# Performance work log

Measured on AMD Instinct MI355X. Metric: run time of the kernel, lower is better.

## Reference

```python
import math
import jax, jax.numpy as jnp
import numpy as np

SR = 48000
FRAME = 240
TWO_PI = 2.0 * math.pi


def _forward(B_inh, f0_offset, A0, tau1, tau2, a1, beat_hz, beat_depth, noise,
             f0, width_factor, duration_s):
    n_samples = int(duration_s * SR)
    T = int(math.ceil(n_samples / FRAME)) * FRAME
    Bb, K = A0.shape

    # --- inharmonic partial frequencies ---
    f0_adj = f0 * 2.0 ** (f0_offset / 1200.0)                      # (B,)
    k = jnp.arange(1, K + 1, dtype=f0.dtype)                       # (K,)
    f_k = f0_adj[:, None] * k[None, :] * jnp.sqrt(1.0 + B_inh[:, None] * k[None, :] ** 2)
    f_kb = f_k + beat_hz                                           # (B,K)

    t = jnp.arange(T, dtype=f0.dtype) / SR                         # (T,)

    # --- two-stage exponential amplitude envelope, (B,K,T) ---
    env = A0[:, :, None] * (a1[:, :, None] * jnp.exp(-t / tau1[:, :, None])
                            + (1.0 - a1[:, :, None]) * jnp.exp(-t / tau2[:, :, None]))

    # fixed random phases (original uses a seeded generator)
    pk = jax.random.split(jax.random.key(42), 3)
    phi_m = jax.random.uniform(pk[0], (Bb, K)) * TWO_PI
    phi_b = jax.random.uniform(pk[1], (Bb, K)) * TWO_PI

    osc = (jnp.cos(TWO_PI * f_k[:, :, None] * t + phi_m[:, :, None])
           + beat_depth[:, :, None] * jnp.cos(TWO_PI * f_kb[:, :, None] * t + phi_b[:, :, None]))

    harmonic = jnp.sum(env * osc, axis=1)                          # (B,T)
    peak = jnp.clip(jnp.max(jnp.abs(harmonic), axis=1, keepdims=True), 1e-6, None)
    harmonic = harmonic / peak * 0.9

    # --- coloured noise: one-pole IIR via parallel associative scan ---
    attack_tau = noise[:, 0:1]                                     # (B,1)
    floor_rms = noise[:, 1:2]                                      # (B,1)
    centroid = noise[:, 2]                                         # (B,)
    nyq = SR / 2.0
    f_lo = 27.5
    log_range = math.log2(nyq / f_lo)
    cutoff = jnp.clip(f_lo * 2.0 ** (centroid * log_range) / nyq, 0.01, 0.99)
    pole = jnp.exp(-TWO_PI * cutoff)                               # (B,)
    alpha = 1.0 - pole

    white = jax.random.normal(pk[2], (Bb, T), dtype=f0.dtype)
    # x_i = pole * x_{i-1} + alpha * w_i  -> affine composition scan over time
    a = jnp.broadcast_to(pole[None, :], (T, Bb))                   # (T,B)
    b = alpha[None, :] * white.T                                   # (T,B)

    def comb(x, y):
        return (x[0] * y[0], x[1] * y[0] + y[1])

    _, filt = jax.lax.associative_scan(comb, (a, b), axis=0)
    noise_env = jnp.exp(-t[None, :] / jnp.clip(attack_tau, 0.002, None)) * floor_rms
    noise_sig = filt.T * noise_env                                 # (B,T)

    mono = (harmonic + noise_sig)[:, :n_samples]
    w = jnp.clip(width_factor, 0.0, 2.0)[:, None]
    side = mono * w * 0.3
    left = jnp.clip(mono + side, -1.0, 1.0)
    right = jnp.clip(mono - side, -1.0, 1.0)
    return jnp.stack([left, right], axis=1)                        # (B,2,n_samples)


def setup_inputs() -> dict:
    key = jax.random.key(0)
    B, K = 4, 64
    ks = jax.random.split(key, 12)
    f0 = jax.random.uniform(ks[0], (B,), minval=65.0, maxval=880.0)
    B_inh = jax.random.uniform(ks[1], (B,)) * 1e-4          # piano inharmonicity
    f0_offset = jax.random.normal(ks[2], (B,)) * 5.0        # cents
    A0 = jax.random.uniform(ks[3], (B, K))
    tau1 = jax.random.uniform(ks[4], (B, K)) * 0.4 + 0.05   # fast decay (s)
    tau2 = jax.random.uniform(ks[5], (B, K)) * 2.0 + 0.5    # slow decay (s)
    a1 = jax.random.uniform(ks[6], (B, K))
    beat_hz = jax.random.uniform(ks[7], (B, K)) * 2.0
    beat_depth = jax.random.uniform(ks[8], (B, K)) * 0.3
    noise = jnp.stack([
        jax.random.uniform(ks[9], (B,)) * 0.1 + 0.01,   # attack_tau
        jax.random.uniform(ks[10], (B,)) * 0.01,        # floor_rms
        jax.random.uniform(ks[11], (B,)),               # centroid_norm
        jnp.zeros((B,)),                                # slope_db_oct (unused)
    ], axis=1)
    width_factor = jnp.ones((B,))
    return dict(B_inh=B_inh, f0_offset=f0_offset, A0=A0, tau1=tau1, tau2=tau2,
                a1=a1, beat_hz=beat_hz, beat_depth=beat_depth, noise=noise,
                f0=f0, width_factor=width_factor, duration_s=3)


def reference(B_inh, f0_offset, A0, tau1, tau2, a1, beat_hz, beat_depth, noise,
              f0, width_factor, duration_s):
    return _forward(B_inh, f0_offset, A0, tau1, tau2, a1, beat_hz, beat_depth,
                    noise, f0, width_factor, duration_s)
```

## Files before the change

### kernel.cpp

```cpp
#include <hip/hip_runtime.h>
#include <stdint.h>
#include <math.h>

#pragma clang fp contract(off)

#define B_BATCH 4
#define K_HARM  64
#define T_TOT   144000
#define N_SAMP  144000
#define WF      128

#define OFF_PK    0
#define PK_STRIDE 16
#define OFF_POLE  4096
#define OFF_ALPHA 4100
#define OFF_AT    4104
#define OFF_FR    4108
#define OFF_WC    4112
#define OFF_PEAK  4116
#define OFF_HARM  4128

static constexpr float  TWO_PI_F = 6.28318530717958647692f;
static constexpr double INV2PI_D = 0.15915494309189535;
static constexpr float  C_HI = (float)INV2PI_D;
static constexpr float  C_LO = (float)(INV2PI_D - (double)((float)INV2PI_D));
static constexpr float  LOG2E_F = 1.44269504088896340736f;
static constexpr float  LN2_F   = 0.69314718055994530942f;

__device__ __forceinline__ uint32_t rotl32(uint32_t x, uint32_t n) {
    return (x << n) | (x >> (32u - n));
}

__device__ __forceinline__ void tf2x32(uint32_t k0, uint32_t k1, uint32_t x0, uint32_t x1,
                                       uint32_t& o0, uint32_t& o1) {
    const uint32_t ks2 = k0 ^ k1 ^ 0x1BD11BDAu;
    x0 += k0; x1 += k1;
#define TF_RND(r) { x0 += x1; x1 = rotl32(x1, (r)); x1 ^= x0; }
    TF_RND(13) TF_RND(15) TF_RND(26) TF_RND(6)
    x0 += k1;  x1 += ks2 + 1u;
    TF_RND(17) TF_RND(29) TF_RND(16) TF_RND(24)
    x0 += ks2; x1 += k0 + 2u;
    TF_RND(13) TF_RND(15) TF_RND(26) TF_RND(6)
    x0 += k0;  x1 += k1 + 3u;
    TF_RND(17) TF_RND(29) TF_RND(16) TF_RND(24)
    x0 += k1;  x1 += ks2 + 4u;
    TF_RND(13) TF_RND(15) TF_RND(26) TF_RND(6)
    x0 += ks2; x1 += k0 + 5u;
#undef TF_RND
    o0 = x0; o1 = x1;
}

__device__ __forceinline__ void get_keys(uint32_t pk[3][2]) {
    tf2x32(0u, 42u, 0u, 0u, pk[0][0], pk[0][1]);
    tf2x32(0u, 42u, 0u, 1u, pk[1][0], pk[1][1]);
    tf2x32(0u, 42u, 0u, 2u, pk[2][0], pk[2][1]);
}

__device__ __forceinline__ uint32_t bits_for(const uint32_t key[2], uint32_t idx) {
    uint32_t o0, o1;
    tf2x32(key[0], key[1], 0u, idx, o0, o1);
    return o0 ^ o1;
}

__device__ __forceinline__ float u01_from_bits(uint32_t bits) {
    return __fsub_rn(__uint_as_float((bits >> 9) | 0x3f800000u), 1.0f);
}

__device__ __forceinline__ float erfinv_fast(float x) {
    float v = fmaf(-x, x, 1.0f);
    float w = __fmul_rn(-LN2_F, __builtin_amdgcn_logf(v));
    float p;
    if (w < 5.0f) {
        w = __fsub_rn(w, 2.5f);
        p = 2.81022636e-08f;
        p = fmaf(p, w, 3.43273939e-07f);
        p = fmaf(p, w, -3.5233877e-06f);
        p = fmaf(p, w, -4.39150654e-06f);
        p = fmaf(p, w, 0.00021858087f);
        p = fmaf(p, w, -0.00125372503f);
        p = fmaf(p, w, -0.00417768164f);
        p = fmaf(p, w, 0.246640727f);
        p = fmaf(p, w, 1.50140941f);
    } else {
        w = __fsub_rn(sqrtf(w), 3.0f);
        p = -0.000200214257f;
        p = fmaf(p, w, 0.000100950558f);
        p = fmaf(p, w, 0.00134934322f);
        p = fmaf(p, w, -0.00367342844f);
        p = fmaf(p, w, 0.00573950773f);
        p = fmaf(p, w, -0.0076224613f);
        p = fmaf(p, w, 0.00943887047f);
        p = fmaf(p, w, 1.00167406f);
        p = fmaf(p, w, 2.83297682f);
    }
    return __fmul_rn(p, x);
}

__device__ __forceinline__ float normal_from_bits(uint32_t bits) {
    const float LO = __uint_as_float(0xBF7FFFFFu);
    float f = u01_from_bits(bits);
    float u = __fadd_rn(__fmul_rn(f, 2.0f), LO);
    u = fmaxf(u, LO);
    const float SQRT2_F = 1.41421356237309504880f;
    return __fmul_rn(SQRT2_F, erfinv_fast(u));
}

__device__ __forceinline__ float reduce_rev(float arg) {
    float p = __fmul_rn(arg, C_HI);
    float e = fmaf(arg, C_HI, -p);
    float n = rintf(p);
    float r = __fadd_rn(__fsub_rn(p, n), e);
    return fmaf(arg, C_LO, r);
}

__global__ void kprep(const float* __restrict__ B_inh, const float* __restrict__ f0_off,
                      const float* __restrict__ beat_hz, const float* __restrict__ noise,
                      const float* __restrict__ f0, const float* __restrict__ wfac,
                      const float* __restrict__ A0, const float* __restrict__ tau1,
                      const float* __restrict__ tau2, const float* __restrict__ a1,
                      const float* __restrict__ bd,
                      float* __restrict__ ws) {
    int j = threadIdx.x;
    uint32_t pk[3][2];
    get_keys(pk);

    float phim = __fmul_rn(u01_from_bits(bits_for(pk[0], (uint32_t)j)), TWO_PI_F);
    float phib = __fmul_rn(u01_from_bits(bits_for(pk[1], (uint32_t)j)), TWO_PI_F);

    int b = j >> 6;
    int k = (j & 63) + 1;
    float x   = __fdiv_rn(f0_off[b], 1200.0f);
    float s   = (float)exp2((double)x);
    float f0a = __fmul_rn(f0[b], s);
    float sq  = sqrtf(__fadd_rn(1.0f, __fmul_rn(B_inh[b], (float)(k * k))));
    float fk  = __fmul_rn(__fmul_rn(f0a, (float)k), sq);
    float fkb = __fadd_rn(fk, beat_hz[j]);

    float w_  = __fmul_rn(TWO_PI_F, fk);
    float wb_ = __fmul_rn(TWO_PI_F, fkb);
    float c1  = __fdiv_rn(-LOG2E_F, __fmul_rn(48000.0f, tau1[j]));
    float c2  = __fdiv_rn(-LOG2E_F, __fmul_rn(48000.0f, tau2[j]));

    float* P = ws + OFF_PK + j * PK_STRIDE;
    P[0] = w_;
    P[1] = wb_;
    P[2] = phim;
    P[3] = phib;
    P[4] = c1;
    P[5] = c2;
    float a1v = a1[j];
    P[6] = __fmul_rn(A0[j], a1v);
    P[7] = __fmul_rn(A0[j], __fsub_rn(1.0f, a1v));
    P[8] = bd[j];
    float revm = __fdiv_rn(fk,  48000.0f); revm = __fsub_rn(revm, floorf(revm));
    float revb = __fdiv_rn(fkb, 48000.0f); revb = __fsub_rn(revb, floorf(revb));
    P[9]  = __builtin_amdgcn_cosf(revm);
    P[10] = __builtin_amdgcn_sinf(revm);
    P[11] = __builtin_amdgcn_cosf(revb);
    P[12] = __builtin_amdgcn_sinf(revb);
    P[13] = __builtin_amdgcn_exp2f(c1);
    P[14] = __builtin_amdgcn_exp2f(c2);

    if (j < B_BATCH) {
        float at  = fmaxf(noise[j * 4 + 0], 0.002f);
        float fr  = noise[j * 4 + 1];
        float cen = noise[j * 4 + 2];
        float lr  = (float)log2(24000.0 / 27.5);
        float y   = __fmul_rn(cen, lr);
        float e   = (float)exp2((double)y);
        float v   = __fdiv_rn(__fmul_rn(27.5f, e), 24000.0f);
        float cut = fminf(fmaxf(v, 0.01f), 0.99f);
        float pole = expf(__fmul_rn(-TWO_PI_F, cut));
        ws[OFF_POLE + j]  = pole;
        ws[OFF_ALPHA + j] = __fsub_rn(1.0f, pole);
        ws[OFF_AT + j] = at;
        ws[OFF_FR + j] = fr;
        ws[OFF_WC + j] = fminf(fmaxf(wfac[j], 0.0f), 2.0f);
        ((unsigned int*)ws)[OFF_PEAK + j] = 0u;
    }
}

#define SPT_H 16
#define TBLK  1024
#define KQ_N  8
#define RROW  1056

__global__ void kharm(const float* __restrict__ prm,
                      float* __restrict__ harm,
                      unsigned int* __restrict__ peak) {
    __shared__ float red[KQ_N][RROW];
    __shared__ float mxs[KQ_N];
    const int tid  = threadIdx.x;
    const int lane = tid & 63;
    const int kq   = __builtin_amdgcn_readfirstlane(tid >> 6);
    const int b    = blockIdx.y;
    const int t0b  = blockIdx.x * TBLK;
    const int t0   = t0b + lane * SPT_H;

    const float fn0 = (float)t0;
    const float tt0 = __fdiv_rn(fn0, 48000.0f);

    float acc[SPT_H];
#pragma unroll
    for (int j = 0; j < SPT_H; ++j) acc[j] = 0.0f;

    const float* Pb = prm + OFF_PK + (((b << 6) + (kq << 3)) * PK_STRIDE);

#pragma unroll 2
    for (int kk = 0; kk < K_HARM / KQ_N; ++kk) {
        const float* P = Pb + kk * PK_STRIDE;
        float w  = P[0], wb2 = P[1], pm = P[2], pb = P[3];
        float c1 = P[4], c2 = P[5], A1 = P[6], A2 = P[7], bdk = P[8];
        float cdm = P[9], sdm = P[10], cdb = P[11], sdb = P[12];
        float d1 = P[13], d2 = P[14];

        float am = __fadd_rn(__fmul_rn(w,   tt0), pm);
        float ab = __fadd_rn(__fmul_rn(wb2, tt0), pb);
        float rm = reduce_rev(am);
        float rb = reduce_rev(ab);
        float cm = __builtin_amdgcn_cosf(rm), sm = __builtin_amdgcn_sinf(rm);
        float cb = __builtin_amdgcn_cosf(rb), sb = __builtin_amdgcn_sinf(rb);

        float xm  = cm;
        float xpm = fmaf(sm, sdm, __fmul_rn(cm, cdm));
        float xb  = __fmul_rn(bdk, cb);
        float xpb = __fmul_rn(bdk, fmaf(sb, sdb, __fmul_rn(cb, cdb)));
        float km  = __fadd_rn(cdm, cdm);
        float kb2 = __fadd_rn(cdb, cdb);
        float e1  = __fmul_rn(A1, __builtin_amdgcn_exp2f(__fmul_rn(fn0, c1)));
        float e2  = __fmul_rn(A2, __builtin_amdgcn_exp2f(__fmul_rn(fn0, c2)));

#pragma unroll
        for (int j = 0; j < SPT_H; ++j) {
            float env = __fadd_rn(e1, e2);
            float osc = __fadd_rn(xm, xb);
            acc[j] = fmaf(env, osc, acc[j]);
            if (j < SPT_H - 1) {
                float xn  = fmaf(km,  xm, -xpm); xpm = xm; xm = xn;
                float xbn = fmaf(kb2, xb, -xpb); xpb = xb; xb = xbn;
                e1 = __fmul_rn(e1, d1);
                e2 = __fmul_rn(e2, d2);
            }
        }
    }

#pragma unroll
    for (int j = 0; j < SPT_H; ++j) {
        int c = lane * SPT_H + j;
        red[kq][c + (c >> 5)] = acc[j];
    }
    __syncthreads();

    int c0  = tid * 2;
    int c1i = c0 + 1;
    int tg  = t0b + c0;
    float m = 0.0f;
    if (tg < T_TOT) {
        float s0 = 0.0f, s1 = 0.0f;
#pragma unroll
        for (int q = 0; q < KQ_N; ++q) {
            s0 = __fadd_rn(s0, red[q][c0  + (c0  >> 5)]);
            s1 = __fadd_rn(s1, red[q][c1i + (c1i >> 5)]);
        }
        *(float2*)(harm + b * T_TOT + tg) = make_float2(s0, s1);
        m = fmaxf(fabsf(s0), fabsf(s1));
    }
#pragma unroll
    for (int off = 32; off > 0; off >>= 1)
        m = fmaxf(m, __shfl_xor(m, off));
    if (lane == 0) mxs[tid >> 6] = m;
    __syncthreads();
    if (tid == 0) {
        float mm = mxs[0];
#pragma unroll
        for (int q = 1; q < KQ_N; ++q) mm = fmaxf(mm, mxs[q]);
        atomicMax(&peak[b], __float_as_uint(mm));
    }
}

#define SPT   4
#define CHUNK 1024
#define WIN   (CHUNK + WF - 1)

__global__ void kfinal(const float* __restrict__ ws, float* __restrict__ out) {
    __shared__ __align__(16) float s[WIN + 1];
    __shared__ __align__(16) float ptab[WF];
    const int b   = blockIdx.y;
    const int t0  = blockIdx.x * CHUNK;
    const int tid = threadIdx.x;

    const float alpha = ws[OFF_ALPHA + b];
    const float pole  = ws[OFF_POLE + b];
    const float at    = ws[OFF_AT + b];
    const float fr    = ws[OFF_FR + b];
    const float wcf   = ws[OFF_WC + b];
    const float peak  = fmaxf(__uint_as_float(((const unsigned int*)ws)[OFF_PEAK + b]), 1e-6f);
    const float cpk   = __fdiv_rn(0.9f, peak);

    uint32_t k2a, k2b;
    tf2x32(0u, 42u, 0u, 2u, k2a, k2b);

    for (int idx = tid; idx < WIN; idx += 256) {
        int j = t0 - (WF - 1) + idx;
        float v = 0.0f;
        if (j >= 0 && j < T_TOT) {
            uint32_t o0, o1;
            tf2x32(k2a, k2b, 0u, (uint32_t)(b * T_TOT + j), o0, o1);
            v = __fmul_rn(alpha, normal_from_bits(o0 ^ o1));
        }
        s[idx] = v;
    }
    if (tid < WF) ptab[tid] = exp2f((float)tid * log2f(pole));
    __syncthreads();

    const int t = t0 + tid * SPT;
    if (t >= N_SAMP) return;
    const float p128 = __fmul_rn(ptab[WF - 1], pole);
    const int base = tid * SPT + (WF - 1);

    float f0 = 0.f, f1 = 0.f, f2 = 0.f, f3 = 0.f;
#pragma unroll
    for (int m4 = 0; m4 < WF / 4; ++m4) {
        float4 p4 = *(const float4*)&ptab[m4 * 4];
        float4 s4 = *(const float4*)&s[base - m4 * 4 - 3];
        f0 = fmaf(p4.x, s4.w, f0);
        f1 = fmaf(p4.y, s4.z, f1);
        f2 = fmaf(p4.z, s4.y, f2);
        f3 = fmaf(p4.w, s4.x, f3);
    }
    float filt = __fadd_rn(__fadd_rn(f0, f2), __fadd_rn(f1, f3));

    const float4 h4 = *(const float4*)(ws + OFF_HARM + b * T_TOT + t);
    float* outL = out + (b * 2 + 0) * N_SAMP;
    float* outR = out + (b * 2 + 1) * N_SAMP;

    float tt  = __fdiv_rn((float)t, 48000.0f);
    float ne  = __fmul_rn(__expf(__fdiv_rn(-tt, at)), fr);
    const float ned = __expf(__fdiv_rn(-1.0f, __fmul_rn(48000.0f, at)));

    const float hv[4] = {h4.x, h4.y, h4.z, h4.w};
    float lv[4], rv[4];
#pragma unroll
    for (int jj = 0; jj < SPT; ++jj) {
        if (jj > 0) {
            filt = fmaf(pole, filt, s[base + jj]);
            filt = fmaf(-p128, s[base + jj - WF], filt);
            ne   = __fmul_rn(ne, ned);
        }
        float hn   = __fmul_rn(hv[jj], cpk);
        float ns   = __fmul_rn(filt, ne);
        float mono = __fadd_rn(hn, ns);
        float side = __fmul_rn(__fmul_rn(mono, wcf), 0.3f);
        lv[jj] = fminf(fmaxf(__fadd_rn(mono, side), -1.0f), 1.0f);
        rv[jj] = fminf(fmaxf(__fsub_rn(mono, side), -1.0f), 1.0f);
    }
    *(float4*)&outL[t] = make_float4(lv[0], lv[1], lv[2], lv[3]);
    *(float4*)&outR[t] = make_float4(rv[0], rv[1], rv[2], rv[3]);
}

extern "C" void kernel_launch(void* const* d_in, const int* in_sizes, int n_in,
                              void* d_out, int out_size, void* d_ws, size_t ws_size,
                              hipStream_t stream) {
    (void)in_sizes; (void)n_in; (void)out_size; (void)ws_size;
    const float* B_inh   = (const float*)d_in[0];
    const float* f0_off  = (const float*)d_in[1];
    const float* A0      = (const float*)d_in[2];
    const float* tau1    = (const float*)d_in[3];
    const float* tau2    = (const float*)d_in[4];
    const float* a1      = (const float*)d_in[5];
    const float* beat_hz = (const float*)d_in[6];
    const float* beat_dp = (const float*)d_in[7];
    const float* noise   = (const float*)d_in[8];
    const float* f0      = (const float*)d_in[9];
    const float* wfac    = (const float*)d_in[10];
    float* out = (float*)d_out;
    float* ws  = (float*)d_ws;

    kprep<<<dim3(1), dim3(256), 0, stream>>>(B_inh, f0_off, beat_hz, noise, f0, wfac,
                                             A0, tau1, tau2, a1, beat_dp, ws);

    dim3 gh((T_TOT + TBLK - 1) / TBLK, B_BATCH);
    kharm<<<gh, dim3(512), 0, stream>>>(ws, ws + OFF_HARM,
                                        (unsigned int*)ws + OFF_PEAK);

    dim3 gf((N_SAMP + CHUNK - 1) / CHUNK, B_BATCH);
    kfinal<<<gf, dim3(256), 0, stream>>>(ws, out);
}
```

Before: 28.73 us.

## Use second-order envelope recurrence and pair harmonics for packed FP32 math

Rewrites the two-exponential envelope as a single second-order linear recurrence, with coefficients d1+d2 and d1*d2 precomputed per partial. This replaces two multiplies plus an add per sample with one fma and one multiply. The harmonic loop now processes two partials together in 2-wide float vectors so the compiler can emit packed FP32 FMA/mul/add instructions, with the two accumulator lanes summed at the end. This costs extra exp2 evaluations for the previous-sample seed and doubles accumulator registers. The recurrence can also drift numerically over the 16-sample run.

```diff
diff --git a/kernel.cpp b/kernel.cpp
--- a/kernel.cpp
+++ b/kernel.cpp
@@ -26,6 +26,15 @@
 static constexpr float  C_LO = (float)(INV2PI_D - (double)((float)INV2PI_D));
 static constexpr float  LOG2E_F = 1.44269504088896340736f;
 static constexpr float  LN2_F   = 0.69314718055994530942f;
+
+typedef float v2f __attribute__((ext_vector_type(2)));
+
+__device__ __forceinline__ v2f pk_fma(v2f a, v2f b, v2f c) {
+    v2f r;
+    r.x = fmaf(a.x, b.x, c.x);
+    r.y = fmaf(a.y, b.y, c.y);
+    return r;
+}
 
 __device__ __forceinline__ uint32_t rotl32(uint32_t x, uint32_t n) {
     return (x << n) | (x >> (32u - n));
@@ -158,8 +167,10 @@
     P[10] = __builtin_amdgcn_sinf(revm);
     P[11] = __builtin_amdgcn_cosf(revb);
     P[12] = __builtin_amdgcn_sinf(revb);
-    P[13] = __builtin_amdgcn_exp2f(c1);
-    P[14] = __builtin_amdgcn_exp2f(c2);
+    float d1 = __builtin_amdgcn_exp2f(c1);
+    float d2 = __builtin_amdgcn_exp2f(c2);
+    P[13] = __fadd_rn(d1, d2);
+    P[14] = __fmul_rn(d1, d2);
 
     if (j < B_BATCH) {
         float at  = fmaxf(noise[j * 4 + 0], 0.002f);
@@ -185,6 +196,39 @@
 #define KQ_N  8
 #define RROW  1056
 
+struct OscInit {
+    float xm, xpm, xb, xpb, km, kb, env, envp, pp, qq;
+};
+
+__device__ __forceinline__ OscInit osc_init(const float* __restrict__ P,
+                                            float tt0, float fn0, float fnm) {
+    float w  = P[0], wb = P[1], pm = P[2], pb = P[3];
+    float c1 = P[4], c2 = P[5], A1 = P[6], A2 = P[7], bdk = P[8];
+    float cdm = P[9], sdm = P[10], cdb = P[11], sdb = P[12];
+    OscInit o;
+    float am = __fadd_rn(__fmul_rn(w,  tt0), pm);
+    float ab = __fadd_rn(__fmul_rn(wb, tt0), pb);
+    float rm = reduce_rev(am);
+    float rb = reduce_rev(ab);
+    float cm = __builtin_amdgcn_cosf(rm), sm = __builtin_amdgcn_sinf(rm);
+    float cb = __builtin_amdgcn_cosf(rb), sb = __builtin_amdgcn_sinf(rb);
+    o.xm  = cm;
+    o.xpm = fmaf(sm, sdm, __fmul_rn(cm, cdm));
+    o.xb  = __fmul_rn(bdk, cb);
+    o.xpb = __fmul_rn(bdk, fmaf(sb, sdb, __fmul_rn(cb, cdb)));
+    o.km  = __fadd_rn(cdm, cdm);
+    o.kb  = __fadd_rn(cdb, cdb);
+    float e1  = __builtin_amdgcn_exp2f(__fmul_rn(fn0, c1));
+    float e2  = __builtin_amdgcn_exp2f(__fmul_rn(fn0, c2));
+    float e1p = __builtin_amdgcn_exp2f(__fmul_rn(fnm, c1));
+    float e2p = __builtin_amdgcn_exp2f(__fmul_rn(fnm, c2));
+    o.env  = fmaf(A1, e1,  __fmul_rn(A2, e2));
+    o.envp = fmaf(A1, e1p, __fmul_rn(A2, e2p));
+    o.pp = P[13];
+    o.qq = P[14];
+    return o;
+}
+
 __global__ void kharm(const float* __restrict__ prm,
                       float* __restrict__ harm,
                       unsigned int* __restrict__ peak) {
@@ -198,48 +242,36 @@
     const int t0   = t0b + lane * SPT_H;
 
     const float fn0 = (float)t0;
+    const float fnm = __fsub_rn(fn0, 1.0f);
     const float tt0 = __fdiv_rn(fn0, 48000.0f);
 
-    float acc[SPT_H];
-#pragma unroll
-    for (int j = 0; j < SPT_H; ++j) acc[j] = 0.0f;
+    v2f ACC[SPT_H];
+#pragma unroll
+    for (int j = 0; j < SPT_H; ++j) ACC[j] = (v2f)0.0f;
 
     const float* Pb = prm + OFF_PK + (((b << 6) + (kq << 3)) * PK_STRIDE);
 
 #pragma unroll 2
-    for (int kk = 0; kk < K_HARM / KQ_N; ++kk) {
-        const float* P = Pb + kk * PK_STRIDE;
-        float w  = P[0], wb2 = P[1], pm = P[2], pb = P[3];
-        float c1 = P[4], c2 = P[5], A1 = P[6], A2 = P[7], bdk = P[8];
-        float cdm = P[9], sdm = P[10], cdb = P[11], sdb = P[12];
-        float d1 = P[13], d2 = P[14];
-
-        float am = __fadd_rn(__fmul_rn(w,   tt0), pm);
-        float ab = __fadd_rn(__fmul_rn(wb2, tt0), pb);
-        float rm = reduce_rev(am);
-        float rb = reduce_rev(ab);
-        float cm = __builtin_amdgcn_cosf(rm), sm = __builtin_amdgcn_sinf(rm);
-        float cb = __builtin_amdgcn_cosf(rb), sb = __builtin_amdgcn_sinf(rb);
-
-        float xm  = cm;
-        float xpm = fmaf(sm, sdm, __fmul_rn(cm, cdm));
-        float xb  = __fmul_rn(bdk, cb);
-        float xpb = __fmul_rn(bdk, fmaf(sb, sdb, __fmul_rn(cb, cdb)));
-        float km  = __fadd_rn(cdm, cdm);
-        float kb2 = __fadd_rn(cdb, cdb);
-        float e1  = __fmul_rn(A1, __builtin_amdgcn_exp2f(__fmul_rn(fn0, c1)));
-        float e2  = __fmul_rn(A2, __builtin_amdgcn_exp2f(__fmul_rn(fn0, c2)));
+    for (int kp = 0; kp < 4; ++kp) {
+        const float* P0 = Pb + (2 * kp) * PK_STRIDE;
+        OscInit oA = osc_init(P0,             tt0, fn0, fnm);
+        OscInit oB = osc_init(P0 + PK_STRIDE, tt0, fn0, fnm);
+
+        v2f XM  = {oA.xm,  oB.xm},  XPM = {oA.xpm, oB.xpm};
+        v2f XB  = {oA.xb,  oB.xb},  XPB = {oA.xpb, oB.xpb};
+        v2f KM  = {oA.km,  oB.km},  KB  = {oA.kb,  oB.kb};
+        v2f ENV = {oA.env, oB.env}, ENVP = {oA.envp, oB.envp};
+        v2f PP  = {oA.pp,  oB.pp},  QQ  = {oA.qq,  oB.qq};
 
 #pragma unroll
         for (int j = 0; j < SPT_H; ++j) {
-            float env = __fadd_rn(e1, e2);
-            float osc = __fadd_rn(xm, xb);
-            acc[j] = fmaf(env, osc, acc[j]);
+            v2f OSC = XM + XB;
+            ACC[j] = pk_fma(ENV, OSC, ACC[j]);
             if (j < SPT_H - 1) {
-                float xn  = fmaf(km,  xm, -xpm); xpm = xm; xm = xn;
-                float xbn = fmaf(kb2, xb, -xpb); xpb = xb; xb = xbn;
-                e1 = __fmul_rn(e1, d1);
-                e2 = __fmul_rn(e2, d2);
+                v2f xn = pk_fma(KM, XM, -XPM); XPM = XM; XM = xn;
+                v2f xb = pk_fma(KB, XB, -XPB); XPB = XB; XB = xb;
+                v2f t  = QQ * ENVP;
+                v2f en = pk_fma(PP, ENV, -t); ENVP = ENV; ENV = en;
             }
         }
     }
@@ -247,7 +279,7 @@
 #pragma unroll
     for (int j = 0; j < SPT_H; ++j) {
         int c = lane * SPT_H + j;
-        red[kq][c + (c >> 5)] = acc[j];
+        red[kq][c + (c >> 5)] = __fadd_rn(ACC[j].x, ACC[j].y);
     }
     __syncthreads();
 
```

Result: no change. 29.13 us (+1.4%).

## Fold parameter prep kernel into harmonic and final kernels, use second-order envelope recurrence

Applied to the files above, without the earlier changes.

Removes the single-block kprep launch: each kharm block recomputes its batch's 64 partial parameters into shared memory, and kfinal recomputes the noise filter coefficients. The peak accumulator is cleared with hipMemsetAsync instead. Separately, the two-exponential envelope is advanced with a single second-order linear recurrence (sum and product of decay factors), replacing two multiplies and an add per sample. This trades a kernel launch and a global-memory round trip for redundant per-block setup work, including Threefry and double-precision exp2, and the recurrence may drift numerically.

```diff
diff --git a/kernel.cpp b/kernel.cpp
--- a/kernel.cpp
+++ b/kernel.cpp
@@ -10,15 +10,8 @@
 #define N_SAMP  144000
 #define WF      128
 
-#define OFF_PK    0
-#define PK_STRIDE 16
-#define OFF_POLE  4096
-#define OFF_ALPHA 4100
-#define OFF_AT    4104
-#define OFF_FR    4108
-#define OFF_WC    4112
-#define OFF_PEAK  4116
-#define OFF_HARM  4128
+#define OFF_PEAK  0
+#define OFF_HARM  64
 
 static constexpr float  TWO_PI_F = 6.28318530717958647692f;
 static constexpr double INV2PI_D = 0.15915494309189535;
@@ -50,15 +43,9 @@
     o0 = x0; o1 = x1;
 }
 
-__device__ __forceinline__ void get_keys(uint32_t pk[3][2]) {
-    tf2x32(0u, 42u, 0u, 0u, pk[0][0], pk[0][1]);
-    tf2x32(0u, 42u, 0u, 1u, pk[1][0], pk[1][1]);
-    tf2x32(0u, 42u, 0u, 2u, pk[2][0], pk[2][1]);
-}
-
-__device__ __forceinline__ uint32_t bits_for(const uint32_t key[2], uint32_t idx) {
+__device__ __forceinline__ uint32_t bits_for_key(uint32_t ka, uint32_t kb, uint32_t idx) {
     uint32_t o0, o1;
-    tf2x32(key[0], key[1], 0u, idx, o0, o1);
+    tf2x32(ka, kb, 0u, idx, o0, o1);
     return o0 ^ o1;
 }
 
@@ -113,81 +100,19 @@
     return fmaf(arg, C_LO, r);
 }
 
-__global__ void kprep(const float* __restrict__ B_inh, const float* __restrict__ f0_off,
-                      const float* __restrict__ beat_hz, const float* __restrict__ noise,
-                      const float* __restrict__ f0, const float* __restrict__ wfac,
-                      const float* __restrict__ A0, const float* __restrict__ tau1,
-                      const float* __restrict__ tau2, const float* __restrict__ a1,
-                      const float* __restrict__ bd,
-                      float* __restrict__ ws) {
-    int j = threadIdx.x;
-    uint32_t pk[3][2];
-    get_keys(pk);
-
-    float phim = __fmul_rn(u01_from_bits(bits_for(pk[0], (uint32_t)j)), TWO_PI_F);
-    float phib = __fmul_rn(u01_from_bits(bits_for(pk[1], (uint32_t)j)), TWO_PI_F);
-
-    int b = j >> 6;
-    int k = (j & 63) + 1;
-    float x   = __fdiv_rn(f0_off[b], 1200.0f);
-    float s   = (float)exp2((double)x);
-    float f0a = __fmul_rn(f0[b], s);
-    float sq  = sqrtf(__fadd_rn(1.0f, __fmul_rn(B_inh[b], (float)(k * k))));
-    float fk  = __fmul_rn(__fmul_rn(f0a, (float)k), sq);
-    float fkb = __fadd_rn(fk, beat_hz[j]);
-
-    float w_  = __fmul_rn(TWO_PI_F, fk);
-    float wb_ = __fmul_rn(TWO_PI_F, fkb);
-    float c1  = __fdiv_rn(-LOG2E_F, __fmul_rn(48000.0f, tau1[j]));
-    float c2  = __fdiv_rn(-LOG2E_F, __fmul_rn(48000.0f, tau2[j]));
-
-    float* P = ws + OFF_PK + j * PK_STRIDE;
-    P[0] = w_;
-    P[1] = wb_;
-    P[2] = phim;
-    P[3] = phib;
-    P[4] = c1;
-    P[5] = c2;
-    float a1v = a1[j];
-    P[6] = __fmul_rn(A0[j], a1v);
-    P[7] = __fmul_rn(A0[j], __fsub_rn(1.0f, a1v));
-    P[8] = bd[j];
-    float revm = __fdiv_rn(fk,  48000.0f); revm = __fsub_rn(revm, floorf(revm));
-    float revb = __fdiv_rn(fkb, 48000.0f); revb = __fsub_rn(revb, floorf(revb));
-    P[9]  = __builtin_amdgcn_cosf(revm);
-    P[10] = __builtin_amdgcn_sinf(revm);
-    P[11] = __builtin_amdgcn_cosf(revb);
-    P[12] = __builtin_amdgcn_sinf(revb);
-    P[13] = __builtin_amdgcn_exp2f(c1);
-    P[14] = __builtin_amdgcn_exp2f(c2);
-
-    if (j < B_BATCH) {
-        float at  = fmaxf(noise[j * 4 + 0], 0.002f);
-        float fr  = noise[j * 4 + 1];
-        float cen = noise[j * 4 + 2];
-        float lr  = (float)log2(24000.0 / 27.5);
-        float y   = __fmul_rn(cen, lr);
-        float e   = (float)exp2((double)y);
-        float v   = __fdiv_rn(__fmul_rn(27.5f, e), 24000.0f);
-        float cut = fminf(fmaxf(v, 0.01f), 0.99f);
-        float pole = expf(__fmul_rn(-TWO_PI_F, cut));
-        ws[OFF_POLE + j]  = pole;
-        ws[OFF_ALPHA + j] = __fsub_rn(1.0f, pole);
-        ws[OFF_AT + j] = at;
-        ws[OFF_FR + j] = fr;
-        ws[OFF_WC + j] = fminf(fmaxf(wfac[j], 0.0f), 2.0f);
-        ((unsigned int*)ws)[OFF_PEAK + j] = 0u;
-    }
-}
-
 #define SPT_H 16
 #define TBLK  1024
 #define KQ_N  8
 #define RROW  1056
-
-__global__ void kharm(const float* __restrict__ prm,
-                      float* __restrict__ harm,
-                      unsigned int* __restrict__ peak) {
+#define PF 16
+
+__global__ void kharm(const float* __restrict__ B_inh, const float* __restrict__ f0_off,
+                      const float* __restrict__ beat_hz, const float* __restrict__ f0,
+                      const float* __restrict__ A0, const float* __restrict__ tau1,
+                      const float* __restrict__ tau2, const float* __restrict__ a1,
+                      const float* __restrict__ bd,
+                      float* __restrict__ harm, unsigned int* __restrict__ peak) {
+    __shared__ float PL[K_HARM][PF];
     __shared__ float red[KQ_N][RROW];
     __shared__ float mxs[KQ_N];
     const int tid  = threadIdx.x;
@@ -197,22 +122,63 @@
     const int t0b  = blockIdx.x * TBLK;
     const int t0   = t0b + lane * SPT_H;
 
+    if (tid < K_HARM) {
+        uint32_t k0a, k0b, k1a, k1b;
+        tf2x32(0u, 42u, 0u, 0u, k0a, k0b);
+        tf2x32(0u, 42u, 0u, 1u, k1a, k1b);
+        int j = (b << 6) + tid;
+        float phim = __fmul_rn(u01_from_bits(bits_for_key(k0a, k0b, (uint32_t)j)), TWO_PI_F);
+        float phib = __fmul_rn(u01_from_bits(bits_for_key(k1a, k1b, (uint32_t)j)), TWO_PI_F);
+
+        int k = tid + 1;
+        float x   = __fdiv_rn(f0_off[b], 1200.0f);
+        float s   = (float)exp2((double)x);
+        float f0a = __fmul_rn(f0[b], s);
+        float sq  = sqrtf(__fadd_rn(1.0f, __fmul_rn(B_inh[b], (float)(k * k))));
+        float fk  = __fmul_rn(__fmul_rn(f0a, (float)k), sq);
+        float fkb = __fadd_rn(fk, beat_hz[j]);
+
+        float c1  = __fdiv_rn(-LOG2E_F, __fmul_rn(48000.0f, tau1[j]));
+        float c2  = __fdiv_rn(-LOG2E_F, __fmul_rn(48000.0f, tau2[j]));
+
+        PL[tid][0] = __fmul_rn(TWO_PI_F, fk);
+        PL[tid][1] = __fmul_rn(TWO_PI_F, fkb);
+        PL[tid][2] = phim;
+        PL[tid][3] = phib;
+        PL[tid][4] = c1;
+        PL[tid][5] = c2;
+        float a1v = a1[j];
+        PL[tid][6] = __fmul_rn(A0[j], a1v);
+        PL[tid][7] = __fmul_rn(A0[j], __fsub_rn(1.0f, a1v));
+        PL[tid][8] = bd[j];
+        float revm = __fdiv_rn(fk,  48000.0f); revm = __fsub_rn(revm, floorf(revm));
+        float revb = __fdiv_rn(fkb, 48000.0f); revb = __fsub_rn(revb, floorf(revb));
+        PL[tid][9]  = __builtin_amdgcn_cosf(revm);
+        PL[tid][10] = __builtin_amdgcn_sinf(revm);
+        PL[tid][11] = __builtin_amdgcn_cosf(revb);
+        PL[tid][12] = __builtin_amdgcn_sinf(revb);
+        float d1 = __builtin_amdgcn_exp2f(c1);
+        float d2 = __builtin_amdgcn_exp2f(c2);
+        PL[tid][13] = __fadd_rn(d1, d2);
+        PL[tid][14] = __fmul_rn(d1, d2);
+    }
+    __syncthreads();
+
     const float fn0 = (float)t0;
+    const float fnm = __fsub_rn(fn0, 1.0f);
     const float tt0 = __fdiv_rn(fn0, 48000.0f);
 
     float acc[SPT_H];
 #pragma unroll
     for (int j = 0; j < SPT_H; ++j) acc[j] = 0.0f;
-
-    const float* Pb = prm + OFF_PK + (((b << 6) + (kq << 3)) * PK_STRIDE);
 
 #pragma unroll 2
     for (int kk = 0; kk < K_HARM / KQ_N; ++kk) {
-        const float* P = Pb + kk * PK_STRIDE;
+        const float* P = PL[(kq << 3) + kk];
         float w  = P[0], wb2 = P[1], pm = P[2], pb = P[3];
         float c1 = P[4], c2 = P[5], A1 = P[6], A2 = P[7], bdk = P[8];
         float cdm = P[9], sdm = P[10], cdb = P[11], sdb = P[12];
-        float d1 = P[13], d2 = P[14];
+        float PP = P[13], QQ = P[14];
 
         float am = __fadd_rn(__fmul_rn(w,   tt0), pm);
         float ab = __fadd_rn(__fmul_rn(wb2, tt0), pb);
@@ -227,19 +193,22 @@
         float xpb = __fmul_rn(bdk, fmaf(sb, sdb, __fmul_rn(cb, cdb)));
         float km  = __fadd_rn(cdm, cdm);
         float kb2 = __fadd_rn(cdb, cdb);
-        float e1  = __fmul_rn(A1, __builtin_amdgcn_exp2f(__fmul_rn(fn0, c1)));
-        float e2  = __fmul_rn(A2, __builtin_amdgcn_exp2f(__fmul_rn(fn0, c2)));
+        float e1  = __builtin_amdgcn_exp2f(__fmul_rn(fn0, c1));
+        float e2  = __builtin_amdgcn_exp2f(__fmul_rn(fn0, c2));
+        float e1p = __builtin_amdgcn_exp2f(__fmul_rn(fnm, c1));
+        float e2p = __builtin_amdgcn_exp2f(__fmul_rn(fnm, c2));
+        float env  = fmaf(A1, e1,  __fmul_rn(A2, e2));
+        float envp = fmaf(A1, e1p, __fmul_rn(A2, e2p));
 
 #pragma unroll
         for (int j = 0; j < SPT_H; ++j) {
-            float env = __fadd_rn(e1, e2);
             float osc = __fadd_rn(xm, xb);
             acc[j] = fmaf(env, osc, acc[j]);
             if (j < SPT_H - 1) {
                 float xn  = fmaf(km,  xm, -xpm); xpm = xm; xm = xn;
                 float xbn = fmaf(kb2, xb, -xpb); xpb = xb; xb = xbn;
-                e1 = __fmul_rn(e1, d1);
-                e2 = __fmul_rn(e2, d2);
+                float tq  = __fmul_rn(QQ, envp);
+                float en  = fmaf(PP, env, -tq); envp = env; env = en;
             }
         }
     }
@@ -282,19 +251,27 @@
 #define CHUNK 1024
 #define WIN   (CHUNK + WF - 1)
 
-__global__ void kfinal(const float* __restrict__ ws, float* __restrict__ out) {
+__global__ void kfinal(const float* __restrict__ noise, const float* __restrict__ wfac,
+                       const float* __restrict__ harm, const unsigned int* __restrict__ peakp,
+                       float* __restrict__ out) {
     __shared__ __align__(16) float s[WIN + 1];
     __shared__ __align__(16) float ptab[WF];
     const int b   = blockIdx.y;
     const int t0  = blockIdx.x * CHUNK;
     const int tid = threadIdx.x;
 
-    const float alpha = ws[OFF_ALPHA + b];
-    const float pole  = ws[OFF_POLE + b];
-    const float at    = ws[OFF_AT + b];
-    const float fr    = ws[OFF_FR + b];
-    const float wcf   = ws[OFF_WC + b];
-    const float peak  = fmaxf(__uint_as_float(((const unsigned int*)ws)[OFF_PEAK + b]), 1e-6f);
+    const float at  = fmaxf(noise[b * 4 + 0], 0.002f);
+    const float fr  = noise[b * 4 + 1];
+    const float cen = noise[b * 4 + 2];
+    const float lr  = (float)log2(24000.0 / 27.5);
+    float y   = __fmul_rn(cen, lr);
+    float e   = (float)exp2((double)y);
+    float v   = __fdiv_rn(__fmul_rn(27.5f, e), 24000.0f);
+    float cut = fminf(fmaxf(v, 0.01f), 0.99f);
+    const float pole  = expf(__fmul_rn(-TWO_PI_F, cut));
+    const float alpha = __fsub_rn(1.0f, pole);
+    const float wcf   = fminf(fmaxf(wfac[b], 0.0f), 2.0f);
+    const float peak  = fmaxf(__uint_as_float(peakp[b]), 1e-6f);
     const float cpk   = __fdiv_rn(0.9f, peak);
 
     uint32_t k2a, k2b;
@@ -302,13 +279,13 @@
 
     for (int idx = tid; idx < WIN; idx += 256) {
         int j = t0 - (WF - 1) + idx;
-        float v = 0.0f;
+        float vv = 0.0f;
         if (j >= 0 && j < T_TOT) {
             uint32_t o0, o1;
             tf2x32(k2a, k2b, 0u, (uint32_t)(b * T_TOT + j), o0, o1);
-            v = __fmul_rn(alpha, normal_from_bits(o0 ^ o1));
+            vv = __fmul_rn(alpha, normal_from_bits(o0 ^ o1));
         }
-        s[idx] = v;
+        s[idx] = vv;
     }
     if (tid < WF) ptab[tid] = exp2f((float)tid * log2f(pole));
     __syncthreads();
@@ -330,7 +307,7 @@
     }
     float filt = __fadd_rn(__fadd_rn(f0, f2), __fadd_rn(f1, f3));
 
-    const float4 h4 = *(const float4*)(ws + OFF_HARM + b * T_TOT + t);
+    const float4 h4 = *(const float4*)(harm + b * T_TOT + t);
     float* outL = out + (b * 2 + 0) * N_SAMP;
     float* outR = out + (b * 2 + 1) * N_SAMP;
 
@@ -376,13 +353,16 @@
     float* out = (float*)d_out;
     float* ws  = (float*)d_ws;
 
-    kprep<<<dim3(1), dim3(256), 0, stream>>>(B_inh, f0_off, beat_hz, noise, f0, wfac,
-                                             A0, tau1, tau2, a1, beat_dp, ws);
+    unsigned int* peak = (unsigned int*)ws + OFF_PEAK;
+    float* harm = ws + OFF_HARM;
+
+    hipMemsetAsync(peak, 0, B_BATCH * sizeof(unsigned int), stream);
 
     dim3 gh((T_TOT + TBLK - 1) / TBLK, B_BATCH);
-    kharm<<<gh, dim3(512), 0, stream>>>(ws, ws + OFF_HARM,
-                                        (unsigned int*)ws + OFF_PEAK);
+    kharm<<<gh, dim3(512), 0, stream>>>(B_inh, f0_off, beat_hz, f0,
+                                        A0, tau1, tau2, a1, beat_dp,
+                                        harm, peak);
 
     dim3 gf((N_SAMP + CHUNK - 1) / CHUNK, B_BATCH);
-    kfinal<<<gf, dim3(256), 0, stream>>>(ws, out);
-}
+    kfinal<<<gf, dim3(256), 0, stream>>>(noise, wfac, harm, peak, out);
+}
```

Result: slower. 29.44 us (+2.5%).
